# Optimization experiments

Hardware: AMD Instinct MI355X
Metric: run time of the kernel (lower is better)

The kernel has to match this reference:

```python
import jax, jax.numpy as jnp
import numpy as np
from jax import lax

SCORE_THRESH = 0.05
NMS_THRESH = 0.5
DETECTIONS_PER_IMG = 100
MIN_SIZE = 0.01
AREA_THRESH = 0.0
BOX_W = (10.0, 10.0, 5.0, 5.0)
BBOX_XFORM_CLIP = float(np.log(1000.0 / 16.0))


def setup_inputs() -> dict:
    key = jax.random.key(0)
    B, N, C = 8, 4000, 91
    H, W = 800, 1333
    k1, k2, k3 = jax.random.split(key, 3)
    # scale logits so a realistic fraction of softmax scores exceed score_thresh
    class_logits = jax.random.normal(k1, (B * N, C), jnp.float32) * 2.0
    box_regression = jax.random.normal(k2, (B * N, C * 4), jnp.float32)
    u = jax.random.uniform(k3, (B, N, 4), jnp.float32)
    x1 = u[..., 0] * (W - 50)
    y1 = u[..., 1] * (H - 50)
    bw = u[..., 2] * 200.0 + 4.0
    bh = u[..., 3] * 200.0 + 4.0
    proposals = jnp.stack([x1, y1, jnp.minimum(x1 + bw, W), jnp.minimum(y1 + bh, H)], axis=-1)
    return {"class_logits": class_logits, "box_regression": box_regression,
            "proposals": proposals, "image_h": H, "image_w": W}


def _decode(rel, props):
    # torchvision BoxCoder.decode: props [P,4], rel [P, C*4] -> [P, C, 4]
    w = props[:, 2] - props[:, 0]
    h = props[:, 3] - props[:, 1]
    cx = props[:, 0] + 0.5 * w
    cy = props[:, 1] + 0.5 * h
    rel = rel.reshape(rel.shape[0], -1, 4)
    dx = rel[..., 0] / BOX_W[0]
    dy = rel[..., 1] / BOX_W[1]
    dw = jnp.minimum(rel[..., 2] / BOX_W[2], BBOX_XFORM_CLIP)
    dh = jnp.minimum(rel[..., 3] / BOX_W[3], BBOX_XFORM_CLIP)
    pcx = dx * w[:, None] + cx[:, None]
    pcy = dy * h[:, None] + cy[:, None]
    pw = jnp.exp(dw) * w[:, None]
    ph = jnp.exp(dh) * h[:, None]
    return jnp.stack([pcx - 0.5 * pw, pcy - 0.5 * ph, pcx + 0.5 * pw, pcy + 0.5 * ph], axis=-1)


def _nms_image(boxes, scores, labels_f, valid, off_unit):
    # greedy batched NMS (class-offset trick) producing first DETECTIONS_PER_IMG survivors
    NEG = -1e9
    s0 = jnp.where(valid, scores, NEG)
    ob = boxes + (labels_f * off_unit)[:, None]  # per-class coordinate offset
    areas = (ob[:, 2] - ob[:, 0]) * (ob[:, 3] - ob[:, 1])

    def step(s, _):
        i = jnp.argmax(s)
        sc = s[i]
        ok = sc > (NEG / 2)
        obi = ob[i]
        ix1 = jnp.maximum(obi[0], ob[:, 0])
        iy1 = jnp.maximum(obi[1], ob[:, 1])
        ix2 = jnp.minimum(obi[2], ob[:, 2])
        iy2 = jnp.minimum(obi[3], ob[:, 3])
        inter = jnp.maximum(ix2 - ix1, 0.0) * jnp.maximum(iy2 - iy1, 0.0)
        ai = (obi[2] - obi[0]) * (obi[3] - obi[1])
        iou = inter / jnp.maximum(ai + areas - inter, 1e-9)
        sup = (iou > NMS_THRESH) & ok
        s = jnp.where(sup, NEG, s).at[i].set(NEG)
        return s, (i, jnp.where(ok, sc, 0.0), ok)

    _, (idx, out_sc, ok) = lax.scan(step, s0, None, length=DETECTIONS_PER_IMG)
    out_boxes = boxes[idx] * ok[:, None]
    out_labels = jnp.where(ok, labels_f[idx], 0.0)
    areas_out = (out_boxes[:, 2] - out_boxes[:, 0]) * (out_boxes[:, 3] - out_boxes[:, 1])
    keep = ok & (areas_out >= AREA_THRESH)
    return out_boxes * keep[:, None], out_sc * keep, jnp.where(keep, out_labels, 0.0), keep


def reference(class_logits, box_regression, proposals, image_h, image_w):
    B, N, _ = proposals.shape
    C = class_logits.shape[-1]
    pred_boxes = _decode(box_regression, proposals.reshape(B * N, 4)).reshape(B, N, C, 4)
    pred_scores = jax.nn.softmax(class_logits, axis=-1).reshape(B, N, C)
    # clip boxes to image
    x = jnp.clip(pred_boxes[..., 0::2], 0.0, float(image_w))
    y = jnp.clip(pred_boxes[..., 1::2], 0.0, float(image_h))
    pred_boxes = jnp.stack([x[..., 0], y[..., 0], x[..., 1], y[..., 1]], axis=-1)
    # drop background class 0, flatten (proposal, class) pairs
    M = N * (C - 1)
    boxes = pred_boxes[:, :, 1:, :].reshape(B, M, 4)
    scores = pred_scores[:, :, 1:].reshape(B, M)
    labels_f = jnp.broadcast_to(jnp.arange(1, C, dtype=boxes.dtype)[None, :], (N, C - 1)).reshape(M)
    ws = boxes[..., 2] - boxes[..., 0]
    hs = boxes[..., 3] - boxes[..., 1]
    valid = (scores > SCORE_THRESH) & (ws >= MIN_SIZE) & (hs >= MIN_SIZE)
    off_unit = float(max(image_h, image_w)) + 1.0
    out_boxes, out_scores, out_labels_f, keep = jax.vmap(
        lambda b, s, v: _nms_image(b, s, labels_f, v, off_unit))(boxes, scores, valid)
    return out_boxes, out_scores, out_labels_f.astype(jnp.int32), keep
```

## Files before the change

kernel.cpp:

```cpp
#include <hip/hip_runtime.h>
#include <stdint.h>

typedef uint32_t u32;
typedef unsigned long long u64;

#define NB 8
#define NPER 4000
#define NC 91
#define NCLS 90
#define NDET 100
#define CHUNKS 64
#define RPB 63
#define LBIN 16
#define PCAP 512
#define BINCAP 512
#define SURVCAP 9216
#define NSFIX (NCLS * NDET)
#define FKCAP 1024
#define VPT 36
#define NBIN 1152
#define SLO 0x3D4CCCCEu
#define SSH 15

__device__ __forceinline__ float4 decode_clip(float4 rel, float w, float h,
                                              float cx, float cy, float W, float H) {
  const float XCLIP = 4.135166556742356f;
  float dx = rel.x / 10.0f;
  float dy = rel.y / 10.0f;
  float dw = fminf(rel.z / 5.0f, XCLIP);
  float dh = fminf(rel.w / 5.0f, XCLIP);
  float qcx = dx * w + cx;
  float qcy = dy * h + cy;
  float qw = expf(dw) * w;
  float qh = expf(dh) * h;
  float x1 = qcx - 0.5f * qw, y1 = qcy - 0.5f * qh;
  float x2 = qcx + 0.5f * qw, y2 = qcy + 0.5f * qh;
  x1 = fminf(fmaxf(x1, 0.0f), W);
  x2 = fminf(fmaxf(x2, 0.0f), W);
  y1 = fminf(fmaxf(y1, 0.0f), H);
  y2 = fminf(fmaxf(y2, 0.0f), H);
  return make_float4(x1, y1, x2, y2);
}

__device__ __forceinline__ u64 rdlane64(u64 v, int sl) {
  u32 lo = (u32)__builtin_amdgcn_readlane((int)(u32)v, sl);
  u32 hi = (u32)__builtin_amdgcn_readlane((int)(u32)(v >> 32), sl);
  return ((u64)hi << 32) | (u64)lo;
}

__device__ __forceinline__ void emit_row(int r, int rl, int lane, float sA, float sB,
    float W, float H, const float4* __restrict__ props4, const float4* __restrict__ breg4,
    u32* s_cnt, u64 (*s_key)[LBIN], float4 (*s_box)[LBIN],
    u32* __restrict__ pc, u64* __restrict__ pk, float4* __restrict__ pb) {
  bool eA_ok = (lane >= 1) && (sA > 0.05f);
  bool eB_ok = (lane < NC - 64) && (sB > 0.05f);
  if (!(eA_ok || eB_ok)) return;
  float4 p = props4[r];
  float w = p.z - p.x, h = p.w - p.y;
  float cx = p.x + 0.5f * w, cy = p.y + 0.5f * h;
  if (eA_ok) {
    float4 raw = decode_clip(breg4[(size_t)r * NC + lane], w, h, cx, cy, W, H);
    if (((raw.z - raw.x) >= 0.01f) && ((raw.w - raw.y) >= 0.01f)) {
      int ci = lane - 1;
      u32 orig = (u32)(rl * NCLS + ci);
      u64 key = ((u64)__float_as_uint(sA) << 22) | (u64)(0x3FFFFFu - orig);
      u32 lp = atomicAdd(&s_cnt[ci], 1u);
      if (lp < LBIN) { s_key[ci][lp] = key; s_box[ci][lp] = raw; }
      else {
        u32 slot = atomicAdd(&pc[ci], 1u);
        if (slot < PCAP) { size_t o = (size_t)ci * PCAP + slot; pk[o] = key; pb[o] = raw; }
      }
    }
  }
  if (eB_ok) {
    float4 raw = decode_clip(breg4[(size_t)r * NC + 64 + lane], w, h, cx, cy, W, H);
    if (((raw.z - raw.x) >= 0.01f) && ((raw.w - raw.y) >= 0.01f)) {
      int ci = 63 + lane;
      u32 orig = (u32)(rl * NCLS + ci);
      u64 key = ((u64)__float_as_uint(sB) << 22) | (u64)(0x3FFFFFu - orig);
      u32 lp = atomicAdd(&s_cnt[ci], 1u);
      if (lp < LBIN) { s_key[ci][lp] = key; s_box[ci][lp] = raw; }
      else {
        u32 slot = atomicAdd(&pc[ci], 1u);
        if (slot < PCAP) { size_t o = (size_t)ci * PCAP + slot; pk[o] = key; pb[o] = raw; }
      }
    }
  }
}

__global__ __launch_bounds__(1024) void k_score(const float* __restrict__ logits,
    const float* __restrict__ boxreg, const float* __restrict__ props,
    const int* __restrict__ dh, const int* __restrict__ dw,
    u32* pool_cnt, u64* pool_key, float4* pool_box) {
  __shared__ u64 s_key[NCLS][LBIN];
  __shared__ float4 s_box[NCLS][LBIN];
  __shared__ u32 s_cnt[NCLS];
  __shared__ u32 s_base[NCLS];
  int tid = threadIdx.x;
  int b = blockIdx.x / CHUNKS;
  int chunk = blockIdx.x % CHUNKS;
  int wave = tid >> 6, lane = tid & 63;
  if (tid < NCLS) s_cnt[tid] = 0u;
  __syncthreads();

  float H = (float)dh[0], W = (float)dw[0];
  const float4* props4 = (const float4*)props;
  const float4* breg4 = (const float4*)boxreg;
  u32* pc = pool_cnt + (size_t)b * NCLS;
  u64* pk = pool_key + (size_t)b * NCLS * PCAP;
  float4* pb = pool_box + (size_t)b * NCLS * PCAP;

  for (int rloc = wave; rloc < RPB; rloc += 32) {
    int rloc1 = rloc + 16;
    int rl0 = chunk * RPB + rloc;
    int rl1 = chunk * RPB + rloc1;
    bool v0 = (rl0 < NPER);
    bool v1 = (rloc1 < RPB) && (rl1 < NPER);
    int r0 = b * NPER + (v0 ? rl0 : 0);
    int r1 = b * NPER + (v1 ? rl1 : 0);
    const float* l0 = logits + (size_t)r0 * NC;
    const float* l1 = logits + (size_t)r1 * NC;
    float xA0 = l0[lane];
    float xA1 = l1[lane];
    float xB0 = (lane < NC - 64) ? l0[64 + lane] : -3.0e38f;
    float xB1 = (lane < NC - 64) ? l1[64 + lane] : -3.0e38f;
    float mx0 = fmaxf(xA0, xB0);
    float mx1 = fmaxf(xA1, xB1);
    for (int o = 32; o; o >>= 1) {
      mx0 = fmaxf(mx0, __shfl_xor(mx0, o));
      mx1 = fmaxf(mx1, __shfl_xor(mx1, o));
    }
    float eA0 = expf(xA0 - mx0);
    float eA1 = expf(xA1 - mx1);
    float eB0 = (lane < NC - 64) ? expf(xB0 - mx0) : 0.0f;
    float eB1 = (lane < NC - 64) ? expf(xB1 - mx1) : 0.0f;
    float sm0 = eA0 + eB0;
    float sm1 = eA1 + eB1;
    for (int o = 32; o; o >>= 1) {
      sm0 += __shfl_xor(sm0, o);
      sm1 += __shfl_xor(sm1, o);
    }
    if (v0) emit_row(r0, rl0, lane, eA0 / sm0, eB0 / sm0, W, H, props4, breg4,
                     s_cnt, s_key, s_box, pc, pk, pb);
    if (v1) emit_row(r1, rl1, lane, eA1 / sm1, eB1 / sm1, W, H, props4, breg4,
                     s_cnt, s_key, s_box, pc, pk, pb);
  }
  __syncthreads();
  if (tid < NCLS) {
    u32 cnt = s_cnt[tid];
    u32 staged = cnt > LBIN ? LBIN : cnt;
    s_base[tid] = staged ? atomicAdd(&pc[tid], staged) : 0u;
  }
  __syncthreads();
  for (int idx = tid; idx < NCLS * LBIN; idx += 1024) {
    int ci = idx / LBIN, j = idx % LBIN;
    u32 cnt = s_cnt[ci];
    u32 staged = cnt > LBIN ? LBIN : cnt;
    if ((u32)j < staged) {
      u32 slot = s_base[ci] + (u32)j;
      if (slot < PCAP) {
        size_t o = (size_t)ci * PCAP + slot;
        pk[o] = s_key[ci][j];
        pb[o] = s_box[ci][j];
      }
    }
  }
}

__global__ __launch_bounds__(256) void k_nms_class(const u32* __restrict__ pool_cnt,
    const u64* __restrict__ pool_key, const float4* __restrict__ pool_box,
    u64* skey, float4* sbox, const int* __restrict__ dh, const int* __restrict__ dw) {
  __shared__ u64 k[BINCAP];
  __shared__ float4 boxu[BINCAP];
  __shared__ u64 ks[BINCAP];
  __shared__ float4 boxs[BINCAP];
  __shared__ float4 s_sb[NDET];
  __shared__ float s_sa[NDET];
  __shared__ u64 s_sk[NDET];
  __shared__ u32 s_sid[NDET];

  int b = blockIdx.x / NCLS;
  int ci = blockIdx.x % NCLS;
  int tid = threadIdx.x;
  u64* outk = skey + (size_t)b * SURVCAP + (size_t)ci * NDET;
  float4* outb = sbox + (size_t)b * SURVCAP + (size_t)ci * NDET;

  u32 cnt = pool_cnt[(size_t)b * NCLS + ci];
  int n = (int)(cnt > PCAP ? PCAP : cnt);
  if (n <= 0) {
    for (int i = tid; i < NDET; i += 256) outk[i] = 0ull;
    return;
  }
  size_t src = ((size_t)b * NCLS + ci) * PCAP;
  for (int i = tid; i < n; i += 256) {
    k[i] = pool_key[src + i];
    boxu[i] = pool_box[src + i];
  }
  __syncthreads();
  for (int i = tid; i < n; i += 256) {
    u64 ki = k[i];
    u32 rank = 0;
    int j = 0;
    for (; j + 4 <= n; j += 4) {
      rank += (k[j] > ki) ? 1u : 0u;
      rank += (k[j + 1] > ki) ? 1u : 0u;
      rank += (k[j + 2] > ki) ? 1u : 0u;
      rank += (k[j + 3] > ki) ? 1u : 0u;
    }
    for (; j < n; ++j) rank += (k[j] > ki) ? 1u : 0u;
    ks[rank] = ki;
    boxs[rank] = boxu[i];
  }
  __syncthreads();
  if (tid >= 64) return;

  float H = (float)dh[0], W = (float)dw[0];
  float loff = (fmaxf(H, W) + 1.0f) * (float)(ci + 1);
  int lane = tid;
  int S = 0;
  for (int base = 0; base < n && S < NDET; base += 64) {
    int i = base + lane;
    bool have = (i < n);
    u64 mykey = 0ull;
    float4 Bb = make_float4(0.f, 0.f, 0.f, 0.f);
    float aB = 0.f;
    if (have) {
      mykey = ks[i];
      float4 raw = boxs[i];
      Bb = make_float4(raw.x + loff, raw.y + loff, raw.z + loff, raw.w + loff);
      aB = (Bb.z - Bb.x) * (Bb.w - Bb.y);
    }
    u64 myword = 0ull;
    int lim = n - base; if (lim > 64) lim = 64;
#pragma unroll 4
    for (int m = 0; m < lim; ++m) {
      float4 As = boxs[base + m];
      float ax = As.x + loff, ay = As.y + loff;
      float az = As.z + loff, aw = As.w + loff;
      float aA = (az - ax) * (aw - ay);
      float ix1 = fmaxf(ax, Bb.x), iy1 = fmaxf(ay, Bb.y);
      float ix2 = fminf(az, Bb.z), iy2 = fminf(aw, Bb.w);
      float inter = fmaxf(ix2 - ix1, 0.0f) * fmaxf(iy2 - iy1, 0.0f);
      float iou = inter / fmaxf(aA + aB - inter, 1e-9f);
      if (iou > 0.5f) myword |= (1ull << m);
    }
    bool alive = have;
    for (int s = 0; s < S; ++s) {
      float4 A = s_sb[s];
      float aA = s_sa[s];
      float ix1 = fmaxf(A.x, Bb.x), iy1 = fmaxf(A.y, Bb.y);
      float ix2 = fminf(A.z, Bb.z), iy2 = fminf(A.w, Bb.w);
      float inter = fmaxf(ix2 - ix1, 0.0f) * fmaxf(iy2 - iy1, 0.0f);
      float iou = inter / fmaxf(aA + aB - inter, 1e-9f);
      if (alive && iou > 0.5f) alive = false;
    }
    u64 mask = __ballot(alive);
    u64 sel = 0ull;
    while (mask != 0ull && S + (int)__popcll(sel) < NDET) {
      int j0 = __builtin_amdgcn_readfirstlane(__builtin_ctzll(mask));
      sel |= (1ull << j0);
      u64 row = rdlane64(myword, j0);
      mask &= ~row;
    }
    if ((sel >> lane) & 1ull) {
      int rank = S + (int)__popcll(sel & ((1ull << lane) - 1ull));
      s_sb[rank] = Bb; s_sa[rank] = aB; s_sk[rank] = mykey; s_sid[rank] = (u32)i;
    }
    S += (int)__popcll(sel);
  }
  for (int i2 = lane; i2 < NDET; i2 += 64) {
    if (i2 < S) {
      outk[i2] = s_sk[i2];
      outb[i2] = boxs[s_sid[i2]];
    } else {
      outk[i2] = 0ull;
    }
  }
}

__global__ __launch_bounds__(256) void k_top(const u64* __restrict__ skey,
    const float4* __restrict__ sbox, float* out) {
  __shared__ u32 hist[NBIN];
  __shared__ u64 fk[FKCAP];
  __shared__ u32 fs[FKCAP];
  __shared__ u64 okey[NDET];
  __shared__ u32 osrc[NDET];
  __shared__ u32 s_cnt[2];
  __shared__ u32 s_bin;

  int b = blockIdx.x;
  int tid = threadIdx.x;
  const u64* kb = skey + (size_t)b * SURVCAP;

  u32 sc[VPT];
#pragma unroll
  for (int v = 0; v < VPT; ++v) {
    u32 j = (u32)tid + (u32)v * 256u;
    sc[v] = (j < NSFIX) ? (u32)(kb[j] >> 22) : 0u;
  }
  for (int i = tid; i < NBIN; i += 256) hist[i] = 0u;
  if (tid == 0) { s_cnt[0] = 0; s_cnt[1] = 0; }
  __syncthreads();

#pragma unroll
  for (int v = 0; v < VPT; ++v) {
    u32 s = sc[v];
    if (s > SLO) atomicAdd(&hist[(s - SLO) >> SSH], 1u);
  }
  __syncthreads();

  if (tid < 64) {
    int lane = tid;
    int base = lane * (NBIN / 64);
    u32 csum = 0;
#pragma unroll
    for (int kk2 = 0; kk2 < NBIN / 64; ++kk2) csum += hist[base + kk2];
    u32 suf = csum;
    for (int o = 1; o < 64; o <<= 1) {
      u32 v = __shfl_down(suf, o);
      if (lane + o < 64) suf += v;
    }
    u64 m = __ballot(suf >= NDET);
    int B = 0;
    if (m) {
      int c = 63 - __builtin_clzll(m);
      u32 rest = (c < 63) ? (u32)__shfl((int)suf, c + 1) : 0u;
      u32 acc = rest;
      int cb = c * (NBIN / 64);
      for (int kk2 = (NBIN / 64) - 1; kk2 >= 0; --kk2) {
        acc += hist[cb + kk2];
        if (acc >= NDET) { B = cb + kk2; break; }
      }
    }
    if (lane == 0) s_bin = (u32)B;
  }
  __syncthreads();
  u32 B = s_bin;

#pragma unroll
  for (int v = 0; v < VPT; ++v) {
    u32 s = sc[v];
    if (s > SLO && ((s - SLO) >> SSH) > B) {
      u32 j = (u32)tid + (u32)v * 256u;
      u32 p = atomicAdd(&s_cnt[0], 1u);
      if (p < FKCAP) { fk[p] = kb[j]; fs[p] = j; }
    }
  }
  __syncthreads();
  if (tid == 0) s_cnt[1] = s_cnt[0];
  __syncthreads();
#pragma unroll
  for (int v = 0; v < VPT; ++v) {
    u32 s = sc[v];
    if (s > SLO && ((s - SLO) >> SSH) == B) {
      u32 j = (u32)tid + (u32)v * 256u;
      u32 p = atomicAdd(&s_cnt[1], 1u);
      if (p < FKCAP) { fk[p] = kb[j]; fs[p] = j; }
    }
  }
  __syncthreads();
  u32 tot = s_cnt[1];
  if (tot > FKCAP) tot = FKCAP;
  if (tid >= 64) return;

  for (int i = tid; i < NDET; i += 64) okey[i] = 0ull;
  for (int i = tid; i < (int)tot; i += 64) {
    u64 ki = fk[i];
    u32 rank = 0;
    for (int j = 0; j < (int)tot; ++j) rank += (fk[j] > ki) ? 1u : 0u;
    if (rank < NDET) { okey[rank] = ki; osrc[rank] = fs[i]; }
  }
  for (int i = tid; i < NDET; i += 64) {
    u64 key = okey[i];
    float b0 = 0.f, b1 = 0.f, b2 = 0.f, b3 = 0.f, sc2 = 0.f, lb = 0.f, kp = 0.f;
    if (key) {
      float4 bx = sbox[(size_t)b * SURVCAP + osrc[i]];
      b0 = bx.x; b1 = bx.y; b2 = bx.z; b3 = bx.w;
      sc2 = __uint_as_float((u32)(key >> 22));
      u32 orig = 0x3FFFFFu - (u32)(key & 0x3FFFFFu);
      lb = (float)(orig % NCLS + 1u);
      kp = 1.0f;
    }
    float* ob = out + ((size_t)b * NDET + i) * 4;
    ob[0] = b0; ob[1] = b1; ob[2] = b2; ob[3] = b3;
    out[NB * NDET * 4 + b * NDET + i] = sc2;
    out[NB * NDET * 5 + b * NDET + i] = lb;
    out[NB * NDET * 6 + b * NDET + i] = kp;
  }
}

extern "C" void kernel_launch(void* const* d_in, const int* in_sizes, int n_in,
                              void* d_out, int out_size, void* d_ws, size_t ws_size,
                              hipStream_t stream) {
  const float* logits = (const float*)d_in[0];
  const float* boxreg = (const float*)d_in[1];
  const float* props  = (const float*)d_in[2];
  const int* dh = (const int*)d_in[3];
  const int* dw = (const int*)d_in[4];
  float* out = (float*)d_out;

  char* ws = (char*)d_ws;
  u32* pool_cnt = (u32*)ws;
  char* p0 = ws + 4096;
  u64* pool_key = (u64*)p0;
  char* p1 = p0 + (size_t)NB * NCLS * PCAP * 8;
  float4* pool_box = (float4*)p1;
  char* p2 = p1 + (size_t)NB * NCLS * PCAP * 16;
  u64* skey = (u64*)p2;
  float4* sbox = (float4*)(p2 + (size_t)NB * SURVCAP * 8);
  (void)ws_size;

  hipMemsetAsync(pool_cnt, 0, (size_t)NB * NCLS * sizeof(u32), stream);

  k_score<<<NB * CHUNKS, 1024, 0, stream>>>(logits, boxreg, props, dh, dw,
                                            pool_cnt, pool_key, pool_box);
  k_nms_class<<<NB * NCLS, 256, 0, stream>>>(pool_cnt, pool_key, pool_box,
                                             skey, sbox, dh, dw);
  k_top<<<NB, 256, 0, stream>>>(skey, sbox, out);
}
```

Measured before the change: 156.9 us.

## Split per-class NMS IoU work across all four wavefronts of the block

The greedy per-class NMS previously ran on a single 64-lane wavefront while the other three waves exited. Now all four waves share the work: each computes a 16-column slice of the intra-chunk IoU bitmask and a strided slice of the checks against already-selected boxes. Results are combined through shared memory, and wave 0 runs the serial selection. This adds two block barriers per 64-box chunk and extra shared-memory traffic in exchange for roughly a quarter of the per-wave IoU work.

After: 150.9 us. 1.04x faster.

```diff
diff --git a/kernel.cpp b/kernel.cpp
--- a/kernel.cpp
+++ b/kernel.cpp
@@ -178,10 +178,14 @@
   __shared__ float s_sa[NDET];
   __shared__ u64 s_sk[NDET];
   __shared__ u32 s_sid[NDET];
+  __shared__ u64 pw[4][64];
+  __shared__ u32 ps[4][64];
+  __shared__ u32 s_S;
 
   int b = blockIdx.x / NCLS;
   int ci = blockIdx.x % NCLS;
   int tid = threadIdx.x;
+  int wv = tid >> 6, lane = tid & 63;
   u64* outk = skey + (size_t)b * SURVCAP + (size_t)ci * NDET;
   float4* outb = sbox + (size_t)b * SURVCAP + (size_t)ci * NDET;
 
@@ -211,69 +215,84 @@
     ks[rank] = ki;
     boxs[rank] = boxu[i];
   }
-  __syncthreads();
-  if (tid >= 64) return;
+  if (tid == 0) s_S = 0u;
+  __syncthreads();
 
   float H = (float)dh[0], W = (float)dw[0];
   float loff = (fmaxf(H, W) + 1.0f) * (float)(ci + 1);
-  int lane = tid;
-  int S = 0;
-  for (int base = 0; base < n && S < NDET; base += 64) {
-    int i = base + lane;
-    bool have = (i < n);
-    u64 mykey = 0ull;
+
+  for (int base = 0; base < n; base += 64) {
+    int S = (int)s_S;
+    if (S >= NDET) break;
+    int lim = n - base; if (lim > 64) lim = 64;
+    bool have = (lane < lim);
     float4 Bb = make_float4(0.f, 0.f, 0.f, 0.f);
     float aB = 0.f;
     if (have) {
-      mykey = ks[i];
-      float4 raw = boxs[i];
+      float4 raw = boxs[base + lane];
       Bb = make_float4(raw.x + loff, raw.y + loff, raw.z + loff, raw.w + loff);
       aB = (Bb.z - Bb.x) * (Bb.w - Bb.y);
     }
-    u64 myword = 0ull;
-    int lim = n - base; if (lim > 64) lim = 64;
-#pragma unroll 4
-    for (int m = 0; m < lim; ++m) {
-      float4 As = boxs[base + m];
-      float ax = As.x + loff, ay = As.y + loff;
-      float az = As.z + loff, aw = As.w + loff;
-      float aA = (az - ax) * (aw - ay);
-      float ix1 = fmaxf(ax, Bb.x), iy1 = fmaxf(ay, Bb.y);
-      float ix2 = fminf(az, Bb.z), iy2 = fminf(aw, Bb.w);
-      float inter = fmaxf(ix2 - ix1, 0.0f) * fmaxf(iy2 - iy1, 0.0f);
-      float iou = inter / fmaxf(aA + aB - inter, 1e-9f);
-      if (iou > 0.5f) myword |= (1ull << m);
-    }
-    bool alive = have;
-    for (int s = 0; s < S; ++s) {
-      float4 A = s_sb[s];
-      float aA = s_sa[s];
-      float ix1 = fmaxf(A.x, Bb.x), iy1 = fmaxf(A.y, Bb.y);
-      float ix2 = fminf(A.z, Bb.z), iy2 = fminf(A.w, Bb.w);
-      float inter = fmaxf(ix2 - ix1, 0.0f) * fmaxf(iy2 - iy1, 0.0f);
-      float iou = inter / fmaxf(aA + aB - inter, 1e-9f);
-      if (alive && iou > 0.5f) alive = false;
-    }
-    u64 mask = __ballot(alive);
-    u64 sel = 0ull;
-    while (mask != 0ull && S + (int)__popcll(sel) < NDET) {
-      int j0 = __builtin_amdgcn_readfirstlane(__builtin_ctzll(mask));
-      sel |= (1ull << j0);
-      u64 row = rdlane64(myword, j0);
-      mask &= ~row;
-    }
-    if ((sel >> lane) & 1ull) {
-      int rank = S + (int)__popcll(sel & ((1ull << lane) - 1ull));
-      s_sb[rank] = Bb; s_sa[rank] = aB; s_sk[rank] = mykey; s_sid[rank] = (u32)i;
-    }
-    S += (int)__popcll(sel);
-  }
-  for (int i2 = lane; i2 < NDET; i2 += 64) {
-    if (i2 < S) {
-      outk[i2] = s_sk[i2];
-      outb[i2] = boxs[s_sid[i2]];
-    } else {
-      outk[i2] = 0ull;
+    u64 w64 = 0ull;
+    if (have) {
+      int m0 = wv << 4, m1 = m0 + 16; if (m1 > lim) m1 = lim;
+      for (int m = m0; m < m1; ++m) {
+        float4 As = boxs[base + m];
+        float ax = As.x + loff, ay = As.y + loff;
+        float az = As.z + loff, aw = As.w + loff;
+        float aA = (az - ax) * (aw - ay);
+        float ix1 = fmaxf(ax, Bb.x), iy1 = fmaxf(ay, Bb.y);
+        float ix2 = fminf(az, Bb.z), iy2 = fminf(aw, Bb.w);
+        float inter = fmaxf(ix2 - ix1, 0.0f) * fmaxf(iy2 - iy1, 0.0f);
+        float iou = inter / fmaxf(aA + aB - inter, 1e-9f);
+        if (iou > 0.5f) w64 |= (1ull << m);
+      }
+    }
+    pw[wv][lane] = w64;
+    u32 f = 0u;
+    if (have) {
+      for (int s = wv; s < S; s += 4) {
+        float4 A = s_sb[s];
+        float aA = s_sa[s];
+        float ix1 = fmaxf(A.x, Bb.x), iy1 = fmaxf(A.y, Bb.y);
+        float ix2 = fminf(A.z, Bb.z), iy2 = fminf(A.w, Bb.w);
+        float inter = fmaxf(ix2 - ix1, 0.0f) * fmaxf(iy2 - iy1, 0.0f);
+        float iou = inter / fmaxf(aA + aB - inter, 1e-9f);
+        if (iou > 0.5f) { f = 1u; break; }
+      }
+    }
+    ps[wv][lane] = f;
+    __syncthreads();
+    if (tid < 64) {
+      u64 myword = pw[0][lane] | pw[1][lane] | pw[2][lane] | pw[3][lane];
+      bool alive = have &&
+                   ((ps[0][lane] | ps[1][lane] | ps[2][lane] | ps[3][lane]) == 0u);
+      u64 mask = __ballot(alive);
+      u64 sel = 0ull;
+      while (mask != 0ull && S + (int)__popcll(sel) < NDET) {
+        int j0 = __builtin_amdgcn_readfirstlane(__builtin_ctzll(mask));
+        sel |= (1ull << j0);
+        u64 row = rdlane64(myword, j0);
+        mask &= ~row;
+      }
+      if ((sel >> lane) & 1ull) {
+        int rank = S + (int)__popcll(sel & ((1ull << lane) - 1ull));
+        s_sb[rank] = Bb; s_sa[rank] = aB;
+        s_sk[rank] = ks[base + lane]; s_sid[rank] = (u32)(base + lane);
+      }
+      if (tid == 0) s_S = (u32)(S + (int)__popcll(sel));
+    }
+    __syncthreads();
+  }
+  if (tid < 64) {
+    int S = (int)s_S;
+    for (int i2 = lane; i2 < NDET; i2 += 64) {
+      if (i2 < S) {
+        outk[i2] = s_sk[i2];
+        outb[i2] = boxs[s_sid[i2]];
+      } else {
+        outk[i2] = 0ull;
+      }
     }
   }
 }
```
